# Kernel optimization log

Measured on AMD Instinct MI355X. Metric: run time of the kernel, lower is better.

The kernel has to match this reference:

```python
import jax, jax.numpy as jnp
import numpy as np

N_HEAD = 16

def setup_inputs() -> dict:
    key = jax.random.key(0)
    ks = jax.random.split(key, 9)
    B, T, C = 2, 2048, 1024
    s = 0.02
    return {
        "x": jax.random.normal(ks[0], (B, T, C), dtype=jnp.float32),
        "Wk": jax.random.normal(ks[1], (C, C), dtype=jnp.float32) * s,
        "bk": jnp.zeros((C,), dtype=jnp.float32),
        "Wq": jax.random.normal(ks[2], (C, C), dtype=jnp.float32) * s,
        "bq": jnp.zeros((C,), dtype=jnp.float32),
        "Wv": jax.random.normal(ks[3], (C, C), dtype=jnp.float32) * s,
        "bv": jnp.zeros((C,), dtype=jnp.float32),
        "Wp": jax.random.normal(ks[4], (C, C), dtype=jnp.float32) * s,
        "bp": jnp.zeros((C,), dtype=jnp.float32),
    }

def reference(x, Wk, bk, Wq, bq, Wv, bv, Wp, bp):
    B, T, C = x.shape
    H = N_HEAD
    D = C // H
    # projections -> [B, H, T, D]
    def split_heads(y):
        return y.reshape(B, T, H, D).transpose(0, 2, 1, 3)
    k = split_heads(x @ Wk.T + bk)
    q = split_heads(x @ Wq.T + bq)
    v = split_heads(x @ Wv.T + bv)
    scale = 1.0 / jnp.sqrt(jnp.asarray(D, dtype=x.dtype))
    att = jnp.einsum("bhtd,bhsd->bhts", q, k) * scale  # [B,H,T,T]
    causal = jnp.tril(jnp.ones((T, T), dtype=bool))
    att = jnp.where(causal, att, jnp.asarray(-jnp.inf, dtype=att.dtype))
    att = jax.nn.softmax(att, axis=-1)
    y = jnp.einsum("bhts,bhsd->bhtd", att, v)  # [B,H,T,D]
    y = y.transpose(0, 2, 1, 3).reshape(B, T, C)
    return y @ Wp.T + bp
```

## Files before the change

### kernel.cpp

```cpp
#include <hip/hip_runtime.h>
#include <stdint.h>

typedef unsigned short u16;
typedef __attribute__((ext_vector_type(8))) short short8;
typedef __attribute__((ext_vector_type(4))) short short4v;
typedef __attribute__((ext_vector_type(4))) float float4v;

#define NB 2
#define NT 2048
#define NC 1024
#define NH 16
#define ND 64
#define NM (NB*NT)

#if defined(__has_builtin)
#if __has_builtin(__builtin_amdgcn_mfma_f32_16x16x16bf16_1k)
#define MFMA16(a, b, c) __builtin_amdgcn_mfma_f32_16x16x16bf16_1k(a, b, c, 0, 0, 0)
#endif
#endif
#ifndef MFMA16
static __device__ __forceinline__ float4v mfma16_asm(short4v a, short4v b, float4v c) {
  asm volatile("v_mfma_f32_16x16x16_bf16 %0, %1, %2, %0" : "+v"(c) : "v"(a), "v"(b));
  return c;
}
#define MFMA16(a, b, c) mfma16_asm(a, b, c)
#endif

#if defined(__has_builtin)
#if __has_builtin(__builtin_amdgcn_exp2f)
#define EXP2(x) __builtin_amdgcn_exp2f(x)
#endif
#endif
#ifndef EXP2
extern "C" __device__ float __ocml_native_exp2_f32(float);
#define EXP2(x) __ocml_native_exp2_f32(x)
#endif

#define WB0 asm volatile("s_waitcnt vmcnt(0)\n\ts_barrier" ::: "memory")
#define BAR_PLAIN asm volatile("s_barrier" ::: "memory")

__device__ __forceinline__ u16 f2bf(float f) {
  union { float f; uint32_t u; } v; v.f = f;
  uint32_t u = v.u;
  u += 0x7fffu + ((u >> 16) & 1u);
  return (u16)(u >> 16);
}
__device__ __forceinline__ float bf2f(u16 u) {
  union { uint32_t u; float f; } v; v.u = ((uint32_t)u) << 16; return v.f;
}

__device__ __forceinline__ short4v pack4bf(float a, float b, float c, float d) {
  union { uint32_t u[2]; short4v s; } r;
  r.u[0] = __builtin_amdgcn_perm(__float_as_uint(b), __float_as_uint(a), 0x07060302u);
  r.u[1] = __builtin_amdgcn_perm(__float_as_uint(d), __float_as_uint(c), 0x07060302u);
  return r.s;
}

__device__ __forceinline__ void gld_lds16(const u16* g, u16* lds) {
  __builtin_amdgcn_global_load_lds(
      (const __attribute__((address_space(1))) uint32_t*)g,
      (__attribute__((address_space(3))) uint32_t*)lds,
      16, 0, 0);
}

__global__ __launch_bounds__(256) void cast_all(
    const float* __restrict__ x,  const float* __restrict__ wk,
    const float* __restrict__ wq, const float* __restrict__ wv,
    const float* __restrict__ wp,
    u16* __restrict__ xb, u16* __restrict__ wkb, u16* __restrict__ wqb,
    u16* __restrict__ wvb, u16* __restrict__ wpb) {
  const int NX = NM * NC / 4;
  const int NW = NC * NC / 4;
  int i = blockIdx.x * 256 + threadIdx.x;
  const float* src; u16* dst; int off;
  if (i < NX)            { src = x;  dst = xb;  off = i; }
  else if (i < NX+NW)    { src = wk; dst = wkb; off = i - NX; }
  else if (i < NX+2*NW)  { src = wq; dst = wqb; off = i - NX - NW; }
  else if (i < NX+3*NW)  { src = wv; dst = wvb; off = i - NX - 2*NW; }
  else if (i < NX+4*NW)  { src = wp; dst = wpb; off = i - NX - 3*NW; }
  else return;
  float4v f = ((const float4v*)src)[off];
  short4v o;
  o.x = (short)f2bf(f.x); o.y = (short)f2bf(f.y);
  o.z = (short)f2bf(f.z); o.w = (short)f2bf(f.w);
  ((short4v*)dst)[off] = o;
}

__global__ __launch_bounds__(256, 2) void qkv_gemm(
    const u16* __restrict__ xb,
    const u16* __restrict__ wqb, const u16* __restrict__ wkb, const u16* __restrict__ wvb,
    const float* __restrict__ bq, const float* __restrict__ bk, const float* __restrict__ bv,
    u16* __restrict__ Q, u16* __restrict__ K, u16* __restrict__ Vt) {
  __shared__ u16 S[4][128 * 64];
  const int id  = blockIdx.x;
  const int mg  = id & 7;
  const int mti = mg * 4 + ((id >> 3) & 3);
  const int rr  = id >> 5;
  const int x8  = rr & 7;
  const int mat = rr >> 3;
  const int n0  = x8 * 128;
  const int m0  = mti * 128;
  const u16*   W    = (mat == 0) ? wqb : (mat == 1) ? wkb : wvb;
  const float* bias = (mat == 0) ? bq  : (mat == 1) ? bk  : bv;

  const int tid = threadIdx.x, wave = tid >> 6, lane = tid & 63;
  const int quad = lane >> 4, l15 = lane & 15;
  const int wm = wave >> 1, wn = wave & 1;

  const u16* A_tile = xb + (size_t)m0 * NC;
  const u16* W_tile = W  + (size_t)n0 * NC;

  const int srow = (lane >> 3);
  const int sgc  = (lane & 7) ^ srow;
  int sOff[4], sLds[4];
#pragma unroll
  for (int ii = 0; ii < 4; ii++) {
    int row_l = ii * 32 + wave * 8 + srow;
    sOff[ii] = row_l * NC + sgc * 8;
    sLds[ii] = (ii * 32 + wave * 8) * 64;
  }

  float4v acc[4][4];
#pragma unroll
  for (int i = 0; i < 4; i++)
#pragma unroll
    for (int j = 0; j < 4; j++) acc[i][j] = (float4v){0.f, 0.f, 0.f, 0.f};

  auto stage = [&](int ki, int p) {
    const u16* a = A_tile + ki * 64;
    const u16* w = W_tile + ki * 64;
#pragma unroll
    for (int ii = 0; ii < 4; ii++) {
      gld_lds16(a + sOff[ii], S[p]     + sLds[ii]);
      gld_lds16(w + sOff[ii], S[2 + p] + sLds[ii]);
    }
  };

  stage(0, 0);
  for (int ki = 0; ki < 16; ki++) {
    const int p = ki & 1;
    WB0;
    if (ki < 15) stage(ki + 1, p ^ 1);
    const u16* As = S[p];
    const u16* Bs = S[2 + p];
#pragma unroll
    for (int kk = 0; kk < 2; kk++) {
      short8 af[4], bf[4];
#pragma unroll
      for (int mt = 0; mt < 4; mt++) {
        int row = wm * 64 + mt * 16 + l15;
        int e   = (kk * 4 + quad) ^ (row & 7);
        af[mt] = *(const short8*)(As + row * 64 + e * 8);
      }
#pragma unroll
      for (int nt = 0; nt < 4; nt++) {
        int row = wn * 64 + nt * 16 + l15;
        int e   = (kk * 4 + quad) ^ (row & 7);
        bf[nt] = *(const short8*)(Bs + row * 64 + e * 8);
      }
#pragma unroll
      for (int mt = 0; mt < 4; mt++)
#pragma unroll
        for (int nt = 0; nt < 4; nt++)
          acc[mt][nt] = __builtin_amdgcn_mfma_f32_16x16x32_bf16(af[mt], bf[nt], acc[mt][nt], 0, 0, 0);
    }
  }

  if (mat != 2) {
    u16* dst = (mat == 0) ? Q : K;
    const float osc = (mat == 0) ? 0.18033688f : 1.0f;
    BAR_PLAIN;
    u16* tile = (u16*)S;
#pragma unroll
    for (int nt = 0; nt < 4; nt++) {
      int col = wn * 64 + nt * 16 + l15;
      float bval = bias[n0 + col];
#pragma unroll
      for (int mt = 0; mt < 4; mt++) {
        int rowb = wm * 64 + mt * 16 + quad * 4;
#pragma unroll
        for (int r = 0; r < 4; r++) {
          int row = rowb + r;
          tile[row * 128 + (col ^ (((row >> 2) & 7) << 4))] =
              f2bf((acc[mt][nt][r] + bval) * osc);
        }
      }
    }
    __syncthreads();
#pragma unroll
    for (int it = 0; it < 8; it++) {
      int idx = it * 256 + tid;
      int row = idx >> 4, ck = idx & 15;
      int s = (row >> 2) & 7;
      short8 v = *(const short8*)(tile + row * 128 + ((((ck >> 1) ^ s) << 4) | ((ck & 1) << 3)));
      *(short8*)(dst + (size_t)(m0 + row) * NC + n0 + ck * 8) = v;
    }
  } else {
    BAR_PLAIN;
    u16* tile = (u16*)S;
#pragma unroll
    for (int nt = 0; nt < 4; nt++) {
      int c = wn * 64 + nt * 16 + l15;
      float bval = bias[n0 + c];
#pragma unroll
      for (int mt = 0; mt < 4; mt++) {
#pragma unroll
        for (int r = 0; r < 4; r++) {
          int mr  = mt * 4 + r;
          int off = wm * 64 + quad * 16 + mr;
          int ck  = (off >> 3) ^ (c & 15);
          tile[c * 128 + ck * 8 + (off & 7)] = f2bf(acc[mt][nt][r] + bval);
        }
      }
    }
    __syncthreads();
    const int b  = m0 >> 11, t0 = m0 & 2047;
    const int bh0 = b * NH + (n0 >> 6);
#pragma unroll
    for (int it = 0; it < 8; it++) {
      int idx = it * 256 + tid;
      int c = idx >> 4, ck = idx & 15;
      short8 v = *(const short8*)(tile + c * 128 + ((ck ^ (c & 15)) * 8));
      *(short8*)(Vt + ((size_t)(bh0 + (c >> 6)) * ND + (c & 63)) * NT + t0 + ck * 8) = v;
    }
  }
}

__global__ __launch_bounds__(256, 4) void attn(
    const u16* __restrict__ Q, const u16* __restrict__ K,
    const u16* __restrict__ Vt, u16* __restrict__ O,
    u16* __restrict__ Opart, float* __restrict__ Lpart) {
  __shared__ u16 Kc[2][64 * 64];
  __shared__ u16 Vc[2][64 * 64];

  const int tid = threadIdx.x, wave = tid >> 6, lane = tid & 63;
  const int quad = lane >> 4, l15 = lane & 15;
  const int c8 = lane & 7, r8 = lane >> 3;
  const int id = blockIdx.x;
  const int gq = (id >> 3) & 31;
  const int gp = id >> 8;
  static const uint8_t QT[8][4] = {
      {15, 16, 4, 0}, {30, 31, 3, 1}, {13, 14, 9, 2}, {25, 26, 10, 5},
      {27, 28, 17, 6}, {29, 11, 18, 7}, {12, 20, 22, 8}, {23, 24, 19, 21}};
  const int cls = QT[gq >> 2][((gq & 3) + gp) & 3];
  const int bh = (id & 7) + 8 * gp;
  const int b = bh >> 4, h = bh & 15;

  int tile, k, c_lo, c_hi, sbase;
  if (cls < 5)        { tile = cls;
                        c_lo = 0; c_hi = 2 * tile + 1; sbase = -1; }
  else if (cls < 17)  { tile = 5 + ((cls - 5) >> 1); k = (cls - 5) & 1;
                        int half = tile + 1;
                        c_lo = k * half; c_hi = c_lo + half - 1;
                        sbase = (tile - 5) * 2 + k; }
  else                { int d3 = cls - 17; int t3 = d3 / 3; k = d3 - 3 * t3;
                        tile = 11 + t3; int C = 2 * tile + 2;
                        c_lo = (k * C) / 3; c_hi = ((k + 1) * C) / 3 - 1;
                        sbase = 12 + t3 * 3 + k; }
  const bool partial = (sbase >= 0);
  const int qb0 = tile * 128 + wave * 32;

  short8 qf[2][2];
#pragma unroll
  for (int j = 0; j < 2; j++) {
    const u16* qrow = Q + (size_t)(b * NT + qb0 + j * 16 + l15) * NC + h * ND + quad * 8;
    qf[j][0] = *(const short8*)(qrow);
    qf[j][1] = *(const short8*)(qrow + 32);
  }

  const short4v vone = {(short)0x3F80, (short)0x3F80, (short)0x3F80, (short)0x3F80};
  float4v l_acc[2];
  float4v o_acc[2][4];
#pragma unroll
  for (int j = 0; j < 2; j++) {
    l_acc[j] = (float4v){0.f, 0.f, 0.f, 0.f};
#pragma unroll
    for (int dt = 0; dt < 4; dt++) o_acc[j][dt] = (float4v){0.f, 0.f, 0.f, 0.f};
  }

  int kOff[2], vOff[2], ldsOff[2];
#pragma unroll
  for (int ii = 0; ii < 2; ii++) {
    int row = wave * 16 + ii * 8 + r8;
    int gc  = c8 ^ (row & 7);
    kOff[ii]   = row * NC + gc * 8;
    vOff[ii]   = row * NT + gc * 8;
    ldsOff[ii] = (wave * 16 + ii * 8) * 64;
  }
  const u16* Kbase = K  + (size_t)b * NT * NC + h * ND;
  const u16* Vbase = Vt + (size_t)bh * ND * NT;

  auto stage = [&](int ci) {
    const int p = (ci - c_lo) & 1;
    const u16* kc = Kbase + (size_t)ci * (64 * NC);
    const u16* vc = Vbase + ci * 64;
#pragma unroll
    for (int ii = 0; ii < 2; ii++) {
      gld_lds16(kc + kOff[ii], Kc[p] + ldsOff[ii]);
      gld_lds16(vc + vOff[ii], Vc[p] + ldsOff[ii]);
    }
  };

  stage(c_lo);
  for (int i = c_lo; i <= c_hi; i++) {
    const int p = (i - c_lo) & 1;
    WB0;
    if (i < c_hi) stage(i + 1);
    if (i * 64 > qb0 + 31) continue;
    const u16* Ks = Kc[p];
    const u16* Vs = Vc[p];
    const bool anymask = (i * 64 + 63) > qb0;
    __builtin_amdgcn_s_setprio(1);

    short4v pf[2][4];
#pragma unroll
    for (int sub = 0; sub < 4; sub++) {
      float4v a0 = (float4v){0.f, 0.f, 0.f, 0.f};
      float4v a1 = (float4v){0.f, 0.f, 0.f, 0.f};
#pragma unroll
      for (int kk = 0; kk < 2; kk++) {
        int row = sub * 16 + l15;
        int ch  = (kk * 4 + quad) ^ (row & 7);
        short8 kf = *(const short8*)(Ks + row * 64 + ch * 8);
        a0 = __builtin_amdgcn_mfma_f32_16x16x32_bf16(kf, qf[0][kk], a0, 0, 0, 0);
        a1 = __builtin_amdgcn_mfma_f32_16x16x32_bf16(kf, qf[1][kk], a1, 0, 0, 0);
      }
      if (!anymask) {
#pragma unroll
        for (int j = 0; j < 2; j++) {
          const float4v& a = (j == 0) ? a0 : a1;
          pf[j][sub] = pack4bf(EXP2(a[0]), EXP2(a[1]), EXP2(a[2]), EXP2(a[3]));
        }
      } else {
#pragma unroll
        for (int j = 0; j < 2; j++) {
          const float4v& a = (j == 0) ? a0 : a1;
          const bool mj = (i * 64 + 63) > (qb0 + j * 16);
          const int qg = qb0 + j * 16 + l15;
          float pv[4];
#pragma unroll
          for (int r = 0; r < 4; r++) {
            float pp = EXP2(a[r]);
            if (mj) {
              int sg = i * 64 + sub * 16 + quad * 4 + r;
              if (sg > qg) pp = 0.f;
            }
            pv[r] = pp;
          }
          pf[j][sub] = pack4bf(pv[0], pv[1], pv[2], pv[3]);
        }
      }
    }

#pragma unroll
    for (int j = 0; j < 2; j++) {
      l_acc[j] = MFMA16(vone, pf[j][0], l_acc[j]);
      l_acc[j] = MFMA16(vone, pf[j][1], l_acc[j]);
      l_acc[j] = MFMA16(vone, pf[j][2], l_acc[j]);
      l_acc[j] = MFMA16(vone, pf[j][3], l_acc[j]);
    }

#pragma unroll
    for (int dt = 0; dt < 4; dt++) {
      int row = dt * 16 + l15;
      int swz = row & 7;
      short8 vA = *(const short8*)(Vs + row * 64 + ((2 * quad)     ^ swz) * 8);
      short8 vB = *(const short8*)(Vs + row * 64 + ((2 * quad + 1) ^ swz) * 8);
      short4v vA0 = __builtin_shufflevector(vA, vA, 0, 1, 2, 3);
      short4v vA1 = __builtin_shufflevector(vA, vA, 4, 5, 6, 7);
      short4v vB0 = __builtin_shufflevector(vB, vB, 0, 1, 2, 3);
      short4v vB1 = __builtin_shufflevector(vB, vB, 4, 5, 6, 7);
#pragma unroll
      for (int j = 0; j < 2; j++) {
        o_acc[j][dt] = MFMA16(vA0, pf[j][0], o_acc[j][dt]);
        o_acc[j][dt] = MFMA16(vA1, pf[j][1], o_acc[j][dt]);
        o_acc[j][dt] = MFMA16(vB0, pf[j][2], o_acc[j][dt]);
        o_acc[j][dt] = MFMA16(vB1, pf[j][3], o_acc[j][dt]);
      }
    }
    __builtin_amdgcn_s_setprio(0);
  }

  float l_tot[2] = {l_acc[0][0], l_acc[1][0]};

  if (!partial) {
#pragma unroll
    for (int j = 0; j < 2; j++) {
      float inv_l = 1.f / l_tot[j];
      const size_t orow = (size_t)(b * NT + qb0 + j * 16 + l15) * NC + h * ND;
#pragma unroll
      for (int dt = 0; dt < 4; dt++)
        *(short4v*)(O + orow + dt * 16 + quad * 4) =
            pack4bf(o_acc[j][dt][0] * inv_l, o_acc[j][dt][1] * inv_l,
                    o_acc[j][dt][2] * inv_l, o_acc[j][dt][3] * inv_l);
    }
  } else {
    const int slab = bh * 27 + sbase;
    u16* ob = Opart + (size_t)slab * 8192;
#pragma unroll
    for (int j = 0; j < 2; j++) {
      const int row = wave * 32 + j * 16 + l15;
#pragma unroll
      for (int dt = 0; dt < 4; dt++)
        *(short4v*)(ob + row * 64 + dt * 16 + quad * 4) =
            pack4bf(o_acc[j][dt][0], o_acc[j][dt][1],
                    o_acc[j][dt][2], o_acc[j][dt][3]);
      if (quad == 0)
        Lpart[slab * 128 + row] = l_tot[j];
    }
  }
}

__global__ __launch_bounds__(256) void combine(
    const u16* __restrict__ Opart, const float* __restrict__ Lp, u16* __restrict__ O) {
  int idx  = blockIdx.x * 256 + threadIdx.x;
  int tIdx = idx >> 10;
  int rem8 = idx & 1023;
  int row  = rem8 >> 3, d0 = (rem8 & 7) * 8;
  int bh   = tIdx / 11;
  int tt   = tIdx - bh * 11;
  int tile = 5 + tt;
  int S, sb;
  if (tile < 11) { S = 2; sb = (tile - 5) * 2; }
  else           { S = 3; sb = 12 + (tile - 11) * 3; }
  int slab0 = bh * 27 + sb;
  float osum[8] = {0.f, 0.f, 0.f, 0.f, 0.f, 0.f, 0.f, 0.f};
  float lsum = 0.f;
  for (int s = 0; s < S; s++) {
    short8 v = *(const short8*)(Opart + (size_t)(slab0 + s) * 8192 + rem8 * 8);
#pragma unroll
    for (int e = 0; e < 8; e++) osum[e] += bf2f((u16)v[e]);
    lsum += Lp[(slab0 + s) * 128 + row];
  }
  float inv = 1.f / lsum;
  short8 o;
#pragma unroll
  for (int e = 0; e < 8; e++) o[e] = (short)f2bf(osum[e] * inv);
  int b = bh >> 4, h = bh & 15;
  int t = tile * 128 + row;
  *(short8*)(O + (size_t)(b * NT + t) * NC + h * ND + d0) = o;
}

__global__ __launch_bounds__(256, 2) void out_gemm(
    const u16* __restrict__ Ob, const u16* __restrict__ wpb,
    const float* __restrict__ bp, float* __restrict__ out) {
  __shared__ u16 Sa[2][64 * 64];
  __shared__ u16 Sb[2][128 * 64];
  const int n0 = blockIdx.x * 128;
  const int m0 = blockIdx.y * 64;
  const int tid = threadIdx.x, wave = tid >> 6, lane = tid & 63;
  const int quad = lane >> 4, l15 = lane & 15;
  const int wm = wave >> 1, wn = wave & 1;

  const u16* A_tile = Ob  + (size_t)m0 * NC;
  const u16* W_tile = wpb + (size_t)n0 * NC;

  const int srow = (lane >> 3);
  const int sgc  = (lane & 7) ^ srow;
  int sOff[4], sLds[4];
#pragma unroll
  for (int ii = 0; ii < 4; ii++) {
    int row_l = ii * 32 + wave * 8 + srow;
    sOff[ii] = row_l * NC + sgc * 8;
    sLds[ii] = (ii * 32 + wave * 8) * 64;
  }

  float4v acc[2][4];
#pragma unroll
  for (int i = 0; i < 2; i++)
#pragma unroll
    for (int j = 0; j < 4; j++) acc[i][j] = (float4v){0.f, 0.f, 0.f, 0.f};

  auto stage = [&](int ki, int p) {
    const u16* a = A_tile + ki * 64;
    const u16* w = W_tile + ki * 64;
#pragma unroll
    for (int ii = 0; ii < 2; ii++)
      gld_lds16(a + sOff[ii], Sa[p] + sLds[ii]);
#pragma unroll
    for (int ii = 0; ii < 4; ii++)
      gld_lds16(w + sOff[ii], Sb[p] + sLds[ii]);
  };

  stage(0, 0);
  for (int ki = 0; ki < 16; ki++) {
    const int p = ki & 1;
    WB0;
    if (ki < 15) stage(ki + 1, p ^ 1);
#pragma unroll
    for (int kk = 0; kk < 2; kk++) {
      short8 af[2], bf[4];
#pragma unroll
      for (int mt = 0; mt < 2; mt++) {
        int row = wm * 32 + mt * 16 + l15;
        int e   = (kk * 4 + quad) ^ (row & 7);
        af[mt] = *(const short8*)(Sa[p] + row * 64 + e * 8);
      }
#pragma unroll
      for (int nt = 0; nt < 4; nt++) {
        int row = wn * 64 + nt * 16 + l15;
        int e   = (kk * 4 + quad) ^ (row & 7);
        bf[nt] = *(const short8*)(Sb[p] + row * 64 + e * 8);
      }
#pragma unroll
      for (int mt = 0; mt < 2; mt++)
#pragma unroll
        for (int nt = 0; nt < 4; nt++)
          acc[mt][nt] = __builtin_amdgcn_mfma_f32_16x16x32_bf16(af[mt], bf[nt], acc[mt][nt], 0, 0, 0);
    }
  }

#pragma unroll
  for (int nt = 0; nt < 4; nt++) {
    int col = n0 + wn * 64 + nt * 16 + l15;
    float bval = bp[col];
#pragma unroll
    for (int mt = 0; mt < 2; mt++) {
      int rowb = m0 + wm * 32 + mt * 16 + quad * 4;
#pragma unroll
      for (int r = 0; r < 4; r++)
        out[(rowb + r) * NC + col] = acc[mt][nt][r] + bval;
    }
  }
}

extern "C" void kernel_launch(void* const* d_in, const int* in_sizes, int n_in,
                              void* d_out, int out_size, void* d_ws, size_t ws_size,
                              hipStream_t stream) {
  const float* x  = (const float*)d_in[0];
  const float* Wk = (const float*)d_in[1];
  const float* bk = (const float*)d_in[2];
  const float* Wq = (const float*)d_in[3];
  const float* bq = (const float*)d_in[4];
  const float* Wv = (const float*)d_in[5];
  const float* bv = (const float*)d_in[6];
  const float* Wp = (const float*)d_in[7];
  const float* bp = (const float*)d_in[8];
  float* out = (float*)d_out;

  uint8_t* ws = (uint8_t*)d_ws;
  const size_t MB = 1u << 20;
  u16* xb    = (u16*)(ws + 0 * MB);
  u16* wkb   = (u16*)(ws + 8 * MB);
  u16* wqb   = (u16*)(ws + 10 * MB);
  u16* wvb   = (u16*)(ws + 12 * MB);
  u16* wpb   = (u16*)(ws + 14 * MB);
  u16* Qb    = (u16*)(ws + 16 * MB);
  u16* Kb    = (u16*)(ws + 24 * MB);
  u16* Vtb   = (u16*)(ws + 32 * MB);
  u16* Ob    = (u16*)(ws + 40 * MB);
  u16* Opart = (u16*)(ws + 0 * MB);
  float* Lpart = (float*)(ws + 13 * MB + 512 * 1024);

  cast_all<<<8192, 256, 0, stream>>>(x, Wk, Wq, Wv, Wp, xb, wkb, wqb, wvb, wpb);
  qkv_gemm<<<768, 256, 0, stream>>>(xb, wqb, wkb, wvb, bq, bk, bv, Qb, Kb, Vtb);
  attn<<<1024, 256, 0, stream>>>(Qb, Kb, Vtb, Ob, Opart, Lpart);
  combine<<<1408, 256, 0, stream>>>(Opart, Lpart, Ob);
  out_gemm<<<dim3(8, 64), 256, 0, stream>>>(Ob, wpb, bp, out);
}
```

Before: 172.8 us.

## Fuse split-KV combine into attention via atomic last-block reduction

Removes the separate combine kernel launch. Each partial attention block writes its slab, bumps a per-tile atomic counter, and the last arriving block reduces the partial outputs and normalizes them in place. The counters are zeroed inside cast_all. This saves one kernel launch and its tail, at the cost of threadfences, an atomic per block, and a serial reduction done by the last block of each tile.

```diff
diff --git a/kernel.cpp b/kernel.cpp
--- a/kernel.cpp
+++ b/kernel.cpp
@@ -68,9 +68,13 @@
     const float* __restrict__ wq, const float* __restrict__ wv,
     const float* __restrict__ wp,
     u16* __restrict__ xb, u16* __restrict__ wkb, u16* __restrict__ wqb,
-    u16* __restrict__ wvb, u16* __restrict__ wpb) {
+    u16* __restrict__ wvb, u16* __restrict__ wpb, int* __restrict__ done) {
   const int NX = NM * NC / 4;
   const int NW = NC * NC / 4;
+  if (blockIdx.x >= 8190) {
+    int t = (blockIdx.x - 8190) * 256 + threadIdx.x;
+    if (t < 352) done[t] = 0;
+  }
   int i = blockIdx.x * 256 + threadIdx.x;
   const float* src; u16* dst; int off;
   if (i < NX)            { src = x;  dst = xb;  off = i; }
@@ -229,9 +233,10 @@
 __global__ __launch_bounds__(256, 4) void attn(
     const u16* __restrict__ Q, const u16* __restrict__ K,
     const u16* __restrict__ Vt, u16* __restrict__ O,
-    u16* __restrict__ Opart, float* __restrict__ Lpart) {
+    u16* __restrict__ Opart, float* __restrict__ Lpart, int* __restrict__ done) {
   __shared__ u16 Kc[2][64 * 64];
   __shared__ u16 Vc[2][64 * 64];
+  __shared__ int lastFlag;
 
   const int tid = threadIdx.x, wave = tid >> 6, lane = tid & 63;
   const int quad = lane >> 4, l15 = lane & 15;
@@ -394,51 +399,52 @@
             pack4bf(o_acc[j][dt][0] * inv_l, o_acc[j][dt][1] * inv_l,
                     o_acc[j][dt][2] * inv_l, o_acc[j][dt][3] * inv_l);
     }
-  } else {
-    const int slab = bh * 27 + sbase;
-    u16* ob = Opart + (size_t)slab * 8192;
-#pragma unroll
-    for (int j = 0; j < 2; j++) {
-      const int row = wave * 32 + j * 16 + l15;
-#pragma unroll
-      for (int dt = 0; dt < 4; dt++)
-        *(short4v*)(ob + row * 64 + dt * 16 + quad * 4) =
-            pack4bf(o_acc[j][dt][0], o_acc[j][dt][1],
-                    o_acc[j][dt][2], o_acc[j][dt][3]);
-      if (quad == 0)
-        Lpart[slab * 128 + row] = l_tot[j];
-    }
-  }
-}
-
-__global__ __launch_bounds__(256) void combine(
-    const u16* __restrict__ Opart, const float* __restrict__ Lp, u16* __restrict__ O) {
-  int idx  = blockIdx.x * 256 + threadIdx.x;
-  int tIdx = idx >> 10;
-  int rem8 = idx & 1023;
-  int row  = rem8 >> 3, d0 = (rem8 & 7) * 8;
-  int bh   = tIdx / 11;
-  int tt   = tIdx - bh * 11;
-  int tile = 5 + tt;
-  int S, sb;
-  if (tile < 11) { S = 2; sb = (tile - 5) * 2; }
-  else           { S = 3; sb = 12 + (tile - 11) * 3; }
-  int slab0 = bh * 27 + sb;
-  float osum[8] = {0.f, 0.f, 0.f, 0.f, 0.f, 0.f, 0.f, 0.f};
-  float lsum = 0.f;
-  for (int s = 0; s < S; s++) {
-    short8 v = *(const short8*)(Opart + (size_t)(slab0 + s) * 8192 + rem8 * 8);
-#pragma unroll
-    for (int e = 0; e < 8; e++) osum[e] += bf2f((u16)v[e]);
-    lsum += Lp[(slab0 + s) * 128 + row];
-  }
-  float inv = 1.f / lsum;
-  short8 o;
-#pragma unroll
-  for (int e = 0; e < 8; e++) o[e] = (short)f2bf(osum[e] * inv);
-  int b = bh >> 4, h = bh & 15;
-  int t = tile * 128 + row;
-  *(short8*)(O + (size_t)(b * NT + t) * NC + h * ND + d0) = o;
+    return;
+  }
+
+  const int slab = bh * 27 + sbase;
+  u16* ob = Opart + (size_t)slab * 8192;
+#pragma unroll
+  for (int j = 0; j < 2; j++) {
+    const int row = wave * 32 + j * 16 + l15;
+#pragma unroll
+    for (int dt = 0; dt < 4; dt++)
+      *(short4v*)(ob + row * 64 + dt * 16 + quad * 4) =
+          pack4bf(o_acc[j][dt][0], o_acc[j][dt][1],
+                  o_acc[j][dt][2], o_acc[j][dt][3]);
+    if (quad == 0)
+      Lpart[slab * 128 + row] = l_tot[j];
+  }
+
+  const int S  = (tile < 11) ? 2 : 3;
+  const int sb = (tile < 11) ? (tile - 5) * 2 : 12 + (tile - 11) * 3;
+  __threadfence();
+  __syncthreads();
+  if (tid == 0) {
+    int prev = atomicAdd(&done[bh * 11 + (tile - 5)], 1);
+    lastFlag = (prev == S - 1);
+  }
+  __syncthreads();
+  if (!lastFlag) return;
+  __threadfence();
+
+  const int slab0 = bh * 27 + sb;
+  for (int q = tid; q < 1024; q += 256) {
+    int row = q >> 3, d0 = (q & 7) * 8;
+    float osum[8] = {0.f, 0.f, 0.f, 0.f, 0.f, 0.f, 0.f, 0.f};
+    float lsum = 0.f;
+    for (int s = 0; s < S; s++) {
+      short8 v = *(const short8*)(Opart + (size_t)(slab0 + s) * 8192 + q * 8);
+#pragma unroll
+      for (int e = 0; e < 8; e++) osum[e] += bf2f((u16)v[e]);
+      lsum += Lpart[(slab0 + s) * 128 + row];
+    }
+    float inv = 1.f / lsum;
+    short8 o;
+#pragma unroll
+    for (int e = 0; e < 8; e++) o[e] = (short)f2bf(osum[e] * inv);
+    *(short8*)(O + (size_t)(b * NT + tile * 128 + row) * NC + h * ND + d0) = o;
+  }
 }
 
 __global__ __launch_bounds__(256, 2) void out_gemm(
@@ -551,10 +557,10 @@
   u16* Ob    = (u16*)(ws + 40 * MB);
   u16* Opart = (u16*)(ws + 0 * MB);
   float* Lpart = (float*)(ws + 13 * MB + 512 * 1024);
-
-  cast_all<<<8192, 256, 0, stream>>>(x, Wk, Wq, Wv, Wp, xb, wkb, wqb, wvb, wpb);
+  int*   done  = (int*)(ws + 48 * MB);
+
+  cast_all<<<8192, 256, 0, stream>>>(x, Wk, Wq, Wv, Wp, xb, wkb, wqb, wvb, wpb, done);
   qkv_gemm<<<768, 256, 0, stream>>>(xb, wqb, wkb, wvb, bq, bk, bv, Qb, Kb, Vtb);
-  attn<<<1024, 256, 0, stream>>>(Qb, Kb, Vtb, Ob, Opart, Lpart);
-  combine<<<1408, 256, 0, stream>>>(Opart, Lpart, Ob);
+  attn<<<1024, 256, 0, stream>>>(Qb, Kb, Vtb, Ob, Opart, Lpart, done);
   out_gemm<<<dim3(8, 64), 256, 0, stream>>>(Ob, wpb, bp, out);
 }
```

After: 335.9 us. 94.4% more time.

## Use 64-row query tiles per block and drop the split-KV combine kernel

Applied to the files above, without the earlier changes.

Attention blocks now each own a 64-query tile (16 rows per wave) covering every KV chunk up to the diagonal. The old design used 128-row tiles with 2- or 3-way KV splits plus a separate combine pass. A new static schedule pairs long and short tiles so blocks stay balanced. The diagonal chunk skips the QK MFMAs for fully masked sub-blocks. This removes the partial-output writes, the combine launch and its reads. In exchange, each K/V chunk loaded into LDS feeds half as many query rows, so K/V traffic per FLOP doubles and MFMA work per LDS read drops.

```diff
diff --git a/kernel.cpp b/kernel.cpp
--- a/kernel.cpp
+++ b/kernel.cpp
@@ -228,8 +228,7 @@
 
 __global__ __launch_bounds__(256, 4) void attn(
     const u16* __restrict__ Q, const u16* __restrict__ K,
-    const u16* __restrict__ Vt, u16* __restrict__ O,
-    u16* __restrict__ Opart, float* __restrict__ Lpart) {
+    const u16* __restrict__ Vt, u16* __restrict__ O) {
   __shared__ u16 Kc[2][64 * 64];
   __shared__ u16 Vc[2][64 * 64];
 
@@ -240,43 +239,26 @@
   const int gq = (id >> 3) & 31;
   const int gp = id >> 8;
   static const uint8_t QT[8][4] = {
-      {15, 16, 4, 0}, {30, 31, 3, 1}, {13, 14, 9, 2}, {25, 26, 10, 5},
-      {27, 28, 17, 6}, {29, 11, 18, 7}, {12, 20, 22, 8}, {23, 24, 19, 21}};
+      {31, 0, 30, 1}, {29, 2, 28, 3}, {27, 4, 26, 5}, {25, 6, 24, 7},
+      {23, 8, 22, 9}, {21, 10, 20, 11}, {19, 12, 18, 13}, {17, 14, 16, 15}};
   const int cls = QT[gq >> 2][((gq & 3) + gp) & 3];
   const int bh = (id & 7) + 8 * gp;
   const int b = bh >> 4, h = bh & 15;
-
-  int tile, k, c_lo, c_hi, sbase;
-  if (cls < 5)        { tile = cls;
-                        c_lo = 0; c_hi = 2 * tile + 1; sbase = -1; }
-  else if (cls < 17)  { tile = 5 + ((cls - 5) >> 1); k = (cls - 5) & 1;
-                        int half = tile + 1;
-                        c_lo = k * half; c_hi = c_lo + half - 1;
-                        sbase = (tile - 5) * 2 + k; }
-  else                { int d3 = cls - 17; int t3 = d3 / 3; k = d3 - 3 * t3;
-                        tile = 11 + t3; int C = 2 * tile + 2;
-                        c_lo = (k * C) / 3; c_hi = ((k + 1) * C) / 3 - 1;
-                        sbase = 12 + t3 * 3 + k; }
-  const bool partial = (sbase >= 0);
-  const int qb0 = tile * 128 + wave * 32;
-
-  short8 qf[2][2];
-#pragma unroll
-  for (int j = 0; j < 2; j++) {
-    const u16* qrow = Q + (size_t)(b * NT + qb0 + j * 16 + l15) * NC + h * ND + quad * 8;
-    qf[j][0] = *(const short8*)(qrow);
-    qf[j][1] = *(const short8*)(qrow + 32);
+  const int qb0 = cls * 64 + wave * 16;
+  const int c_hi = cls;
+
+  short8 qf[2];
+  {
+    const u16* qrow = Q + (size_t)(b * NT + qb0 + l15) * NC + h * ND + quad * 8;
+    qf[0] = *(const short8*)(qrow);
+    qf[1] = *(const short8*)(qrow + 32);
   }
 
   const short4v vone = {(short)0x3F80, (short)0x3F80, (short)0x3F80, (short)0x3F80};
-  float4v l_acc[2];
-  float4v o_acc[2][4];
-#pragma unroll
-  for (int j = 0; j < 2; j++) {
-    l_acc[j] = (float4v){0.f, 0.f, 0.f, 0.f};
-#pragma unroll
-    for (int dt = 0; dt < 4; dt++) o_acc[j][dt] = (float4v){0.f, 0.f, 0.f, 0.f};
-  }
+  float4v l_acc = (float4v){0.f, 0.f, 0.f, 0.f};
+  float4v o_acc[4];
+#pragma unroll
+  for (int dt = 0; dt < 4; dt++) o_acc[dt] = (float4v){0.f, 0.f, 0.f, 0.f};
 
   int kOff[2], vOff[2], ldsOff[2];
 #pragma unroll
@@ -291,7 +273,7 @@
   const u16* Vbase = Vt + (size_t)bh * ND * NT;
 
   auto stage = [&](int ci) {
-    const int p = (ci - c_lo) & 1;
+    const int p = ci & 1;
     const u16* kc = Kbase + (size_t)ci * (64 * NC);
     const u16* vc = Vbase + ci * 64;
 #pragma unroll
@@ -301,64 +283,49 @@
     }
   };
 
-  stage(c_lo);
-  for (int i = c_lo; i <= c_hi; i++) {
-    const int p = (i - c_lo) & 1;
+  stage(0);
+  for (int i = 0; i <= c_hi; i++) {
+    const int p = i & 1;
     WB0;
     if (i < c_hi) stage(i + 1);
-    if (i * 64 > qb0 + 31) continue;
     const u16* Ks = Kc[p];
     const u16* Vs = Vc[p];
-    const bool anymask = (i * 64 + 63) > qb0;
+    const bool diag = (i == c_hi);
     __builtin_amdgcn_s_setprio(1);
 
-    short4v pf[2][4];
+    short4v pf[4];
 #pragma unroll
     for (int sub = 0; sub < 4; sub++) {
-      float4v a0 = (float4v){0.f, 0.f, 0.f, 0.f};
-      float4v a1 = (float4v){0.f, 0.f, 0.f, 0.f};
-#pragma unroll
-      for (int kk = 0; kk < 2; kk++) {
-        int row = sub * 16 + l15;
-        int ch  = (kk * 4 + quad) ^ (row & 7);
-        short8 kf = *(const short8*)(Ks + row * 64 + ch * 8);
-        a0 = __builtin_amdgcn_mfma_f32_16x16x32_bf16(kf, qf[0][kk], a0, 0, 0, 0);
-        a1 = __builtin_amdgcn_mfma_f32_16x16x32_bf16(kf, qf[1][kk], a1, 0, 0, 0);
-      }
-      if (!anymask) {
-#pragma unroll
-        for (int j = 0; j < 2; j++) {
-          const float4v& a = (j == 0) ? a0 : a1;
-          pf[j][sub] = pack4bf(EXP2(a[0]), EXP2(a[1]), EXP2(a[2]), EXP2(a[3]));
+      if (!diag || sub <= wave) {
+        float4v a = (float4v){0.f, 0.f, 0.f, 0.f};
+#pragma unroll
+        for (int kk = 0; kk < 2; kk++) {
+          int row = sub * 16 + l15;
+          int ch  = (kk * 4 + quad) ^ (row & 7);
+          short8 kf = *(const short8*)(Ks + row * 64 + ch * 8);
+          a = __builtin_amdgcn_mfma_f32_16x16x32_bf16(kf, qf[kk], a, 0, 0, 0);
+        }
+        if (diag && sub == wave) {
+          float pv[4];
+#pragma unroll
+          for (int r = 0; r < 4; r++) {
+            float pp = EXP2(a[r]);
+            if ((quad * 4 + r) > l15) pp = 0.f;
+            pv[r] = pp;
+          }
+          pf[sub] = pack4bf(pv[0], pv[1], pv[2], pv[3]);
+        } else {
+          pf[sub] = pack4bf(EXP2(a[0]), EXP2(a[1]), EXP2(a[2]), EXP2(a[3]));
         }
       } else {
-#pragma unroll
-        for (int j = 0; j < 2; j++) {
-          const float4v& a = (j == 0) ? a0 : a1;
-          const bool mj = (i * 64 + 63) > (qb0 + j * 16);
-          const int qg = qb0 + j * 16 + l15;
-          float pv[4];
-#pragma unroll
-          for (int r = 0; r < 4; r++) {
-            float pp = EXP2(a[r]);
-            if (mj) {
-              int sg = i * 64 + sub * 16 + quad * 4 + r;
-              if (sg > qg) pp = 0.f;
-            }
-            pv[r] = pp;
-          }
-          pf[j][sub] = pack4bf(pv[0], pv[1], pv[2], pv[3]);
-        }
-      }
-    }
-
-#pragma unroll
-    for (int j = 0; j < 2; j++) {
-      l_acc[j] = MFMA16(vone, pf[j][0], l_acc[j]);
-      l_acc[j] = MFMA16(vone, pf[j][1], l_acc[j]);
-      l_acc[j] = MFMA16(vone, pf[j][2], l_acc[j]);
-      l_acc[j] = MFMA16(vone, pf[j][3], l_acc[j]);
-    }
+        pf[sub] = (short4v){0, 0, 0, 0};
+      }
+    }
+
+    l_acc = MFMA16(vone, pf[0], l_acc);
+    l_acc = MFMA16(vone, pf[1], l_acc);
+    l_acc = MFMA16(vone, pf[2], l_acc);
+    l_acc = MFMA16(vone, pf[3], l_acc);
 
 #pragma unroll
     for (int dt = 0; dt < 4; dt++) {
@@ -370,75 +337,21 @@
       short4v vA1 = __builtin_shufflevector(vA, vA, 4, 5, 6, 7);
       short4v vB0 = __builtin_shufflevector(vB, vB, 0, 1, 2, 3);
       short4v vB1 = __builtin_shufflevector(vB, vB, 4, 5, 6, 7);
-#pragma unroll
-      for (int j = 0; j < 2; j++) {
-        o_acc[j][dt] = MFMA16(vA0, pf[j][0], o_acc[j][dt]);
-        o_acc[j][dt] = MFMA16(vA1, pf[j][1], o_acc[j][dt]);
-        o_acc[j][dt] = MFMA16(vB0, pf[j][2], o_acc[j][dt]);
-        o_acc[j][dt] = MFMA16(vB1, pf[j][3], o_acc[j][dt]);
-      }
+      o_acc[dt] = MFMA16(vA0, pf[0], o_acc[dt]);
+      o_acc[dt] = MFMA16(vA1, pf[1], o_acc[dt]);
+      o_acc[dt] = MFMA16(vB0, pf[2], o_acc[dt]);
+      o_acc[dt] = MFMA16(vB1, pf[3], o_acc[dt]);
     }
     __builtin_amdgcn_s_setprio(0);
   }
 
-  float l_tot[2] = {l_acc[0][0], l_acc[1][0]};
-
-  if (!partial) {
-#pragma unroll
-    for (int j = 0; j < 2; j++) {
-      float inv_l = 1.f / l_tot[j];
-      const size_t orow = (size_t)(b * NT + qb0 + j * 16 + l15) * NC + h * ND;
-#pragma unroll
-      for (int dt = 0; dt < 4; dt++)
-        *(short4v*)(O + orow + dt * 16 + quad * 4) =
-            pack4bf(o_acc[j][dt][0] * inv_l, o_acc[j][dt][1] * inv_l,
-                    o_acc[j][dt][2] * inv_l, o_acc[j][dt][3] * inv_l);
-    }
-  } else {
-    const int slab = bh * 27 + sbase;
-    u16* ob = Opart + (size_t)slab * 8192;
-#pragma unroll
-    for (int j = 0; j < 2; j++) {
-      const int row = wave * 32 + j * 16 + l15;
-#pragma unroll
-      for (int dt = 0; dt < 4; dt++)
-        *(short4v*)(ob + row * 64 + dt * 16 + quad * 4) =
-            pack4bf(o_acc[j][dt][0], o_acc[j][dt][1],
-                    o_acc[j][dt][2], o_acc[j][dt][3]);
-      if (quad == 0)
-        Lpart[slab * 128 + row] = l_tot[j];
-    }
-  }
-}
-
-__global__ __launch_bounds__(256) void combine(
-    const u16* __restrict__ Opart, const float* __restrict__ Lp, u16* __restrict__ O) {
-  int idx  = blockIdx.x * 256 + threadIdx.x;
-  int tIdx = idx >> 10;
-  int rem8 = idx & 1023;
-  int row  = rem8 >> 3, d0 = (rem8 & 7) * 8;
-  int bh   = tIdx / 11;
-  int tt   = tIdx - bh * 11;
-  int tile = 5 + tt;
-  int S, sb;
-  if (tile < 11) { S = 2; sb = (tile - 5) * 2; }
-  else           { S = 3; sb = 12 + (tile - 11) * 3; }
-  int slab0 = bh * 27 + sb;
-  float osum[8] = {0.f, 0.f, 0.f, 0.f, 0.f, 0.f, 0.f, 0.f};
-  float lsum = 0.f;
-  for (int s = 0; s < S; s++) {
-    short8 v = *(const short8*)(Opart + (size_t)(slab0 + s) * 8192 + rem8 * 8);
-#pragma unroll
-    for (int e = 0; e < 8; e++) osum[e] += bf2f((u16)v[e]);
-    lsum += Lp[(slab0 + s) * 128 + row];
-  }
-  float inv = 1.f / lsum;
-  short8 o;
-#pragma unroll
-  for (int e = 0; e < 8; e++) o[e] = (short)f2bf(osum[e] * inv);
-  int b = bh >> 4, h = bh & 15;
-  int t = tile * 128 + row;
-  *(short8*)(O + (size_t)(b * NT + t) * NC + h * ND + d0) = o;
+  float inv_l = 1.f / l_acc[0];
+  const size_t orow = (size_t)(b * NT + qb0 + l15) * NC + h * ND;
+#pragma unroll
+  for (int dt = 0; dt < 4; dt++)
+    *(short4v*)(O + orow + dt * 16 + quad * 4) =
+        pack4bf(o_acc[dt][0] * inv_l, o_acc[dt][1] * inv_l,
+                o_acc[dt][2] * inv_l, o_acc[dt][3] * inv_l);
 }
 
 __global__ __launch_bounds__(256, 2) void out_gemm(
@@ -549,12 +462,9 @@
   u16* Kb    = (u16*)(ws + 24 * MB);
   u16* Vtb   = (u16*)(ws + 32 * MB);
   u16* Ob    = (u16*)(ws + 40 * MB);
-  u16* Opart = (u16*)(ws + 0 * MB);
-  float* Lpart = (float*)(ws + 13 * MB + 512 * 1024);
 
   cast_all<<<8192, 256, 0, stream>>>(x, Wk, Wq, Wv, Wp, xb, wkb, wqb, wvb, wpb);
   qkv_gemm<<<768, 256, 0, stream>>>(xb, wqb, wkb, wvb, bq, bk, bv, Qb, Kb, Vtb);
-  attn<<<1024, 256, 0, stream>>>(Qb, Kb, Vtb, Ob, Opart, Lpart);
-  combine<<<1408, 256, 0, stream>>>(Opart, Lpart, Ob);
+  attn<<<1024, 256, 0, stream>>>(Qb, Kb, Vtb, Ob);
   out_gemm<<<dim3(8, 64), 256, 0, stream>>>(Ob, wpb, bp, out);
 }
```

Measured after the change: 169.9 us. Within noise of the previous version (-1.7%).
